# Kernel tuning notes

Measured on AMD Instinct MI355X. Metric: run time of the kernel, lower is better.

## Reference

```python
import jax, jax.numpy as jnp
import numpy as np

N, DEG, F, H, O, B = 100000, 16, 128, 128, 128, 8192


def setup_inputs() -> dict:
    key = jax.random.key(0)
    k1, k2, k3, k4, k5 = jax.random.split(key, 5)
    features = jax.random.normal(k1, (N, F), dtype=jnp.float32)
    w1 = jax.random.normal(k2, (2 * F, H), dtype=jnp.float32)
    w2 = jax.random.normal(k3, (2 * H, O), dtype=jnp.float32)
    neighbor_idx = jax.random.randint(k4, (N, DEG), 0, N, dtype=jnp.int32)
    nodes = jax.random.randint(k5, (B,), 0, N, dtype=jnp.int32)
    return {"features": features, "w1": w1, "w2": w2,
            "neighbor_idx": neighbor_idx, "nodes": nodes}


def reference(features, w1, w2, neighbor_idx, nodes):
    # Layer 1 (computed for all nodes, vectorized): mean-aggregate neighbor
    # raw features, concat with self features, project with w1.
    neigh_feat = features[neighbor_idx]                 # [N, DEG, F] gather
    agg1 = neigh_feat.mean(axis=1)                      # [N, F]
    h1 = jnp.concatenate([features, agg1], axis=-1) @ w1  # [N, H]

    # Layer 2 (batch nodes): mean-aggregate neighbor layer-1 embeddings,
    # concat with self layer-1 embedding, project with w2.
    h1_self = h1[nodes]                                 # [B, H]
    h1_neigh = h1[neighbor_idx[nodes]].mean(axis=1)     # [B, H]
    out = jnp.concatenate([h1_self, h1_neigh], axis=-1) @ w2  # [B, O]
    return out
```

## Files before the change

### kernel.cpp

```cpp
#include <hip/hip_runtime.h>


#define N_NODES 100000
#define DEG     16
#define FDIM    128
#define HDIM    128
#define B_NODES 8192

typedef __attribute__((ext_vector_type(8))) short bf16x8;
typedef __attribute__((ext_vector_type(8))) unsigned short u16x8;
typedef __attribute__((ext_vector_type(4))) float f32x4;
typedef __attribute__((ext_vector_type(2))) float f32x2;

static __device__ __forceinline__ unsigned short f2bf(float f) {
    union { float f; unsigned u; } v; v.f = f;
    unsigned r = v.u + 0x7fff + ((v.u >> 16) & 1);
    return (unsigned short)(r >> 16);
}
static __device__ __forceinline__ float bf2f(unsigned short b) {
    union { unsigned u; float f; } v; v.u = ((unsigned)b) << 16;
    return v.f;
}

__global__ __launch_bounds__(256)
void prep(const float* __restrict__ feat, const float* __restrict__ w1,
          const float* __restrict__ w2, unsigned short* __restrict__ fb,
          unsigned char* __restrict__ f8,
          unsigned short* __restrict__ w1T, unsigned short* __restrict__ w2T) {
    if (blockIdx.x < 6250) {
        long e = ((long)blockIdx.x * 256 + threadIdx.x) * 8;
        float4 v0 = *(const float4*)(feat + e);
        float4 v1 = *(const float4*)(feat + e + 4);
        u16x8 ob;
        ob[0] = f2bf(v0.x); ob[1] = f2bf(v0.y); ob[2] = f2bf(v0.z); ob[3] = f2bf(v0.w);
        ob[4] = f2bf(v1.x); ob[5] = f2bf(v1.y); ob[6] = f2bf(v1.z); ob[7] = f2bf(v1.w);
        *(u16x8*)(fb + e) = ob;
        int p0 = 0, p1 = 0;
        p0 = __builtin_amdgcn_cvt_pk_fp8_f32(v0.x, v0.y, p0, false);
        p0 = __builtin_amdgcn_cvt_pk_fp8_f32(v0.z, v0.w, p0, true);
        p1 = __builtin_amdgcn_cvt_pk_fp8_f32(v1.x, v1.y, p1, false);
        p1 = __builtin_amdgcn_cvt_pk_fp8_f32(v1.z, v1.w, p1, true);
        uint2 o8; o8.x = (unsigned)p0; o8.y = (unsigned)p1;
        *(uint2*)(f8 + e) = o8;
    } else {
        int bid = blockIdx.x - 6250;
        const float* w = (bid < 8) ? w1 : w2;
        unsigned short* wT = (bid < 8) ? w1T : w2T;
        int kb = (bid & 7) * 32;
        int n = threadIdx.x & 127, dk = threadIdx.x >> 7;
#pragma unroll
        for (int i = 0; i < 16; ++i) {
            int k = kb + dk * 16 + i;
            wT[n * 256 + k] = f2bf(w[k * 128 + n]);
        }
    }
}

__global__ __launch_bounds__(256)
void k1_agg(const unsigned char* __restrict__ f8, const int* __restrict__ nbr,
            unsigned short* __restrict__ agg) {
    const int t = threadIdx.x;
    const int node = blockIdx.x * 16 + (t >> 4);
    const int cg = (t & 15) * 8;
    const int* idx = nbr + node * DEG;
    int4 i0 = *(const int4*)(idx);
    int4 i1 = *(const int4*)(idx + 4);
    int4 i2 = *(const int4*)(idx + 8);
    int4 i3 = *(const int4*)(idx + 12);
    int id[16] = {i0.x, i0.y, i0.z, i0.w, i1.x, i1.y, i1.z, i1.w,
                  i2.x, i2.y, i2.z, i2.w, i3.x, i3.y, i3.z, i3.w};
    uint2 v[16];
#pragma unroll
    for (int d = 0; d < DEG; ++d)
        v[d] = *(const uint2*)(f8 + (long)id[d] * FDIM + cg);
    float s[8] = {0.f, 0.f, 0.f, 0.f, 0.f, 0.f, 0.f, 0.f};
#pragma unroll
    for (int d = 0; d < DEG; ++d) {
        f32x2 a0 = __builtin_amdgcn_cvt_pk_f32_fp8((int)v[d].x, false);
        f32x2 a1 = __builtin_amdgcn_cvt_pk_f32_fp8((int)v[d].x, true);
        f32x2 a2 = __builtin_amdgcn_cvt_pk_f32_fp8((int)v[d].y, false);
        f32x2 a3 = __builtin_amdgcn_cvt_pk_f32_fp8((int)v[d].y, true);
        s[0] += a0[0]; s[1] += a0[1]; s[2] += a1[0]; s[3] += a1[1];
        s[4] += a2[0]; s[5] += a2[1]; s[6] += a3[0]; s[7] += a3[1];
    }
    u16x8 o;
#pragma unroll
    for (int j = 0; j < 8; ++j) o[j] = f2bf(s[j] * 0.0625f);
    *(u16x8*)(agg + node * 128 + cg) = o;
}

#define LOAD_CHUNK(BUF, CIDX)                                                        \
    do {                                                                             \
        const int r0_ = row0 + (CIDX) * 32;                                          \
        _Pragma("unroll")                                                            \
        for (int mt_ = 0; mt_ < 2; ++mt_) {                                          \
            int grow_ = r0_ + mt_ * 16 + m16;                                        \
            bool ok_ = grow_ < N_NODES;                                              \
            const unsigned short* pf_ = fb + (long)grow_ * 128 + quad * 8;           \
            const unsigned short* pa_ = agg + (long)grow_ * 128 + quad * 8;          \
            bf16x8 z_ = {};                                                          \
            _Pragma("unroll")                                                        \
            for (int kc_ = 0; kc_ < 4; ++kc_)                                        \
                BUF[mt_][kc_] = ok_ ? *(const bf16x8*)(pf_ + kc_ * 32) : z_;         \
            _Pragma("unroll")                                                        \
            for (int kc_ = 0; kc_ < 4; ++kc_)                                        \
                BUF[mt_][4 + kc_] = ok_ ? *(const bf16x8*)(pa_ + kc_ * 32) : z_;     \
        }                                                                            \
    } while (0)

__global__ __launch_bounds__(256, 2)
void g1(const unsigned short* __restrict__ fb, const unsigned short* __restrict__ agg,
        const unsigned short* __restrict__ w1T, unsigned short* __restrict__ h1) {
    __shared__ unsigned short W[128][264];
    const int t = threadIdx.x, wave = t >> 6, lane = t & 63;
    const int m16 = lane & 15, quad = lane >> 4;
    const int row0 = blockIdx.x * 256;
    const int n0 = wave * 32;

#pragma unroll
    for (int i = 0; i < 16; ++i) {
        int e = i * 2048 + t * 8;
        int n = e >> 8, k = e & 255;
        *(u16x8*)(&W[n][k]) = *(const u16x8*)(w1T + e);
    }
    __syncthreads();

    bf16x8 A0[2][8], A1[2][8], A2[2][8];
    LOAD_CHUNK(A0, 0);
    LOAD_CHUNK(A1, 1);

#pragma unroll
    for (int c = 0; c < 8; ++c) {
        if (c < 6) {
            if ((c % 3) == 0)      LOAD_CHUNK(A2, c + 2);
            else if ((c % 3) == 1) LOAD_CHUNK(A0, c + 2);
            else                   LOAD_CHUNK(A1, c + 2);
        }
        f32x4 acc[2][2] = {};
#pragma unroll
        for (int kc = 0; kc < 8; ++kc) {
            bf16x8 b0 = *(const bf16x8*)(&W[n0 + m16][kc * 32 + quad * 8]);
            bf16x8 b1 = *(const bf16x8*)(&W[n0 + 16 + m16][kc * 32 + quad * 8]);
            bf16x8 a0, a1;
            if ((c % 3) == 0)      { a0 = A0[0][kc]; a1 = A0[1][kc]; }
            else if ((c % 3) == 1) { a0 = A1[0][kc]; a1 = A1[1][kc]; }
            else                   { a0 = A2[0][kc]; a1 = A2[1][kc]; }
            acc[0][0] = __builtin_amdgcn_mfma_f32_16x16x32_bf16(a0, b0, acc[0][0], 0, 0, 0);
            acc[1][0] = __builtin_amdgcn_mfma_f32_16x16x32_bf16(a1, b0, acc[1][0], 0, 0, 0);
            acc[0][1] = __builtin_amdgcn_mfma_f32_16x16x32_bf16(a0, b1, acc[0][1], 0, 0, 0);
            acc[1][1] = __builtin_amdgcn_mfma_f32_16x16x32_bf16(a1, b1, acc[1][1], 0, 0, 0);
        }
        const int r0 = row0 + c * 32;
#pragma unroll
        for (int mt = 0; mt < 2; ++mt)
#pragma unroll
            for (int reg = 0; reg < 4; ++reg) {
                int grow = r0 + mt * 16 + quad * 4 + reg;
                if (grow >= N_NODES) continue;
#pragma unroll
                for (int nt = 0; nt < 2; ++nt)
                    h1[grow * HDIM + n0 + nt * 16 + m16] = f2bf(acc[mt][nt][reg]);
            }
    }
}

__global__ __launch_bounds__(256)
void g2_fused(const unsigned short* __restrict__ h1, const unsigned short* __restrict__ w2T,
              const int* __restrict__ nbr, const int* __restrict__ nodes,
              float* __restrict__ out) {
    __shared__ unsigned short X2[64][264];
    const int t = threadIdx.x, wave = t >> 6, lane = t & 63;
    const int m16 = lane & 15, quad = lane >> 4;
    const int b0 = blockIdx.x * 64;
    const int colb = m16 * 8;

    for (int g = 0; g < 4; ++g) {
        int Ln = wave * 16 + g * 4 + quad;
        int node = nodes[b0 + Ln];
        *(u16x8*)(&X2[Ln][colb]) = *(const u16x8*)(h1 + node * HDIM + colb);
        const int* idx = nbr + node * DEG;
        float s[8] = {0.f, 0.f, 0.f, 0.f, 0.f, 0.f, 0.f, 0.f};
#pragma unroll
        for (int d = 0; d < DEG; ++d) {
            int nb = idx[d];
            u16x8 v = *(const u16x8*)(h1 + nb * HDIM + colb);
#pragma unroll
            for (int j = 0; j < 8; ++j) s[j] += bf2f(v[j]);
        }
        u16x8 o;
#pragma unroll
        for (int j = 0; j < 8; ++j) o[j] = f2bf(s[j] * 0.0625f);
        *(u16x8*)(&X2[Ln][128 + colb]) = o;
    }
    __syncthreads();

    f32x4 acc[8] = {};
#pragma unroll
    for (int kc = 0; kc < 8; ++kc) {
        bf16x8 a = *(const bf16x8*)(&X2[wave * 16 + m16][kc * 32 + quad * 8]);
#pragma unroll
        for (int nt = 0; nt < 8; ++nt) {
            bf16x8 b = *(const bf16x8*)(w2T + (nt * 16 + m16) * 256 + kc * 32 + quad * 8);
            acc[nt] = __builtin_amdgcn_mfma_f32_16x16x32_bf16(a, b, acc[nt], 0, 0, 0);
        }
    }

#pragma unroll
    for (int nt = 0; nt < 8; ++nt)
#pragma unroll
        for (int reg = 0; reg < 4; ++reg) {
            int row = b0 + wave * 16 + quad * 4 + reg;
            out[row * 128 + nt * 16 + m16] = acc[nt][reg];
        }
}

extern "C" void kernel_launch(void* const* d_in, const int* in_sizes, int n_in,
                              void* d_out, int out_size, void* d_ws, size_t ws_size,
                              hipStream_t stream) {
    const float* feat  = (const float*)d_in[0];
    const float* w1    = (const float*)d_in[1];
    const float* w2    = (const float*)d_in[2];
    const int*   nbr   = (const int*)d_in[3];
    const int*   nodes = (const int*)d_in[4];
    float* out = (float*)d_out;

    char* ws = (char*)d_ws;
    unsigned short* fb  = (unsigned short*)ws;
    unsigned char*  f8  = (unsigned char*)(ws + 25600000);
    unsigned short* agg = (unsigned short*)(ws + 38400000);
    unsigned short* h1  = (unsigned short*)(ws + 64000000);
    unsigned short* w1T = (unsigned short*)(ws + 89600000);
    unsigned short* w2T = (unsigned short*)(ws + 89665536);

    prep<<<6266, 256, 0, stream>>>(feat, w1, w2, fb, f8, w1T, w2T);
    k1_agg<<<6250, 256, 0, stream>>>(f8, nbr, agg);
    g1<<<(N_NODES + 255) / 256, 256, 0, stream>>>(fb, agg, w1T, h1);
    g2_fused<<<B_NODES / 64, 256, 0, stream>>>(h1, w2T, nbr, nodes, out);
}
```

Measured before the change: 193.9 us.

## Slice fp8 features by column and restage g1 GEMM through LDS

Prep now writes the fp8 feature copy as four 32-column slices, and k1_agg is remapped so that groups of blocks gather from a single slice. This shrinks the gather working set per slice so it fits better in cache. Separately, g1 is rewritten to use 128-row tiles, with A and W K-chunks streamed into double-buffered LDS via global_load_lds and each wave computing the full 128-column output. The new g1 syncs once per K step and reloads W per chunk instead of keeping it resident in LDS, and g1 rows past N_NODES are read without bounds guards.

```diff
diff --git a/kernel.cpp b/kernel.cpp
--- a/kernel.cpp
+++ b/kernel.cpp
@@ -25,7 +25,7 @@
 __global__ __launch_bounds__(256)
 void prep(const float* __restrict__ feat, const float* __restrict__ w1,
           const float* __restrict__ w2, unsigned short* __restrict__ fb,
-          unsigned char* __restrict__ f8,
+          unsigned char* __restrict__ f8s,
           unsigned short* __restrict__ w1T, unsigned short* __restrict__ w2T) {
     if (blockIdx.x < 6250) {
         long e = ((long)blockIdx.x * 256 + threadIdx.x) * 8;
@@ -40,8 +40,11 @@
         p0 = __builtin_amdgcn_cvt_pk_fp8_f32(v0.z, v0.w, p0, true);
         p1 = __builtin_amdgcn_cvt_pk_fp8_f32(v1.x, v1.y, p1, false);
         p1 = __builtin_amdgcn_cvt_pk_fp8_f32(v1.z, v1.w, p1, true);
+        int node = (int)(e >> 7), col = (int)(e & 127);
+        int slice = col >> 5;
+        unsigned char* dst = f8s + (long)slice * (N_NODES * 32) + (long)node * 32 + (col & 31);
         uint2 o8; o8.x = (unsigned)p0; o8.y = (unsigned)p1;
-        *(uint2*)(f8 + e) = o8;
+        *(uint2*)dst = o8;
     } else {
         int bid = blockIdx.x - 6250;
         const float* w = (bid < 8) ? w1 : w2;
@@ -57,11 +60,15 @@
 }
 
 __global__ __launch_bounds__(256)
-void k1_agg(const unsigned char* __restrict__ f8, const int* __restrict__ nbr,
+void k1_agg(const unsigned char* __restrict__ f8s, const int* __restrict__ nbr,
             unsigned short* __restrict__ agg) {
-    const int t = threadIdx.x;
-    const int node = blockIdx.x * 16 + (t >> 4);
-    const int cg = (t & 15) * 8;
+    const int t = threadIdx.x, b = blockIdx.x;
+    const int s = (b & 7) >> 1;
+    const int chunk = ((b >> 3) << 1) + (b & 1);
+    const int node = chunk * 64 + (t >> 2);
+    if (node >= N_NODES) return;
+    const int q = t & 3;
+    const unsigned char* base = f8s + (long)s * (N_NODES * 32) + q * 8;
     const int* idx = nbr + node * DEG;
     int4 i0 = *(const int4*)(idx);
     int4 i1 = *(const int4*)(idx + 4);
@@ -72,96 +79,89 @@
     uint2 v[16];
 #pragma unroll
     for (int d = 0; d < DEG; ++d)
-        v[d] = *(const uint2*)(f8 + (long)id[d] * FDIM + cg);
-    float s[8] = {0.f, 0.f, 0.f, 0.f, 0.f, 0.f, 0.f, 0.f};
+        v[d] = *(const uint2*)(base + (long)id[d] * 32);
+    float sm[8] = {0.f, 0.f, 0.f, 0.f, 0.f, 0.f, 0.f, 0.f};
 #pragma unroll
     for (int d = 0; d < DEG; ++d) {
         f32x2 a0 = __builtin_amdgcn_cvt_pk_f32_fp8((int)v[d].x, false);
         f32x2 a1 = __builtin_amdgcn_cvt_pk_f32_fp8((int)v[d].x, true);
         f32x2 a2 = __builtin_amdgcn_cvt_pk_f32_fp8((int)v[d].y, false);
         f32x2 a3 = __builtin_amdgcn_cvt_pk_f32_fp8((int)v[d].y, true);
-        s[0] += a0[0]; s[1] += a0[1]; s[2] += a1[0]; s[3] += a1[1];
-        s[4] += a2[0]; s[5] += a2[1]; s[6] += a3[0]; s[7] += a3[1];
+        sm[0] += a0[0]; sm[1] += a0[1]; sm[2] += a1[0]; sm[3] += a1[1];
+        sm[4] += a2[0]; sm[5] += a2[1]; sm[6] += a3[0]; sm[7] += a3[1];
     }
     u16x8 o;
 #pragma unroll
-    for (int j = 0; j < 8; ++j) o[j] = f2bf(s[j] * 0.0625f);
-    *(u16x8*)(agg + node * 128 + cg) = o;
-}
-
-#define LOAD_CHUNK(BUF, CIDX)                                                        \
-    do {                                                                             \
-        const int r0_ = row0 + (CIDX) * 32;                                          \
-        _Pragma("unroll")                                                            \
-        for (int mt_ = 0; mt_ < 2; ++mt_) {                                          \
-            int grow_ = r0_ + mt_ * 16 + m16;                                        \
-            bool ok_ = grow_ < N_NODES;                                              \
-            const unsigned short* pf_ = fb + (long)grow_ * 128 + quad * 8;           \
-            const unsigned short* pa_ = agg + (long)grow_ * 128 + quad * 8;          \
-            bf16x8 z_ = {};                                                          \
-            _Pragma("unroll")                                                        \
-            for (int kc_ = 0; kc_ < 4; ++kc_)                                        \
-                BUF[mt_][kc_] = ok_ ? *(const bf16x8*)(pf_ + kc_ * 32) : z_;         \
-            _Pragma("unroll")                                                        \
-            for (int kc_ = 0; kc_ < 4; ++kc_)                                        \
-                BUF[mt_][4 + kc_] = ok_ ? *(const bf16x8*)(pa_ + kc_ * 32) : z_;     \
-        }                                                                            \
+    for (int j = 0; j < 8; ++j) o[j] = f2bf(sm[j] * 0.0625f);
+    *(u16x8*)(agg + (long)node * 128 + s * 32 + q * 8) = o;
+}
+
+#define STAGE(KC, BUF)                                                                        \
+    do {                                                                                      \
+        const unsigned short* s0_ = ((KC) < 4) ? (fb + (KC) * 32) : (agg + ((KC) - 4) * 32);  \
+        _Pragma("unroll")                                                                     \
+        for (int j_ = 0; j_ < 2; ++j_) {                                                      \
+            long grow_ = row0 + (t >> 2) + j_ * 64;                                           \
+            const unsigned short* ga_ = s0_ + grow_ * 128 + (t & 3) * 8;                      \
+            __builtin_amdgcn_global_load_lds(                                                 \
+                (const __attribute__((address_space(1))) unsigned int*)ga_,                   \
+                (__attribute__((address_space(3))) unsigned int*)                             \
+                    (&AsS[(BUF) * 4096 + wave * 512 + j_ * 2048 + lane * 8]), 16, 0, 0);      \
+            const unsigned short* gw_ = w1T + ((t >> 2) + j_ * 64) * 256 + (KC) * 32 + (t & 3) * 8; \
+            __builtin_amdgcn_global_load_lds(                                                 \
+                (const __attribute__((address_space(1))) unsigned int*)gw_,                   \
+                (__attribute__((address_space(3))) unsigned int*)                             \
+                    (&WsS[(BUF) * 4096 + wave * 512 + j_ * 2048 + lane * 8]), 16, 0, 0);      \
+        }                                                                                     \
     } while (0)
 
 __global__ __launch_bounds__(256, 2)
 void g1(const unsigned short* __restrict__ fb, const unsigned short* __restrict__ agg,
         const unsigned short* __restrict__ w1T, unsigned short* __restrict__ h1) {
-    __shared__ unsigned short W[128][264];
+    __shared__ unsigned short AsS[2 * 4096];
+    __shared__ unsigned short WsS[2 * 4096];
     const int t = threadIdx.x, wave = t >> 6, lane = t & 63;
     const int m16 = lane & 15, quad = lane >> 4;
-    const int row0 = blockIdx.x * 256;
-    const int n0 = wave * 32;
-
-#pragma unroll
-    for (int i = 0; i < 16; ++i) {
-        int e = i * 2048 + t * 8;
-        int n = e >> 8, k = e & 255;
-        *(u16x8*)(&W[n][k]) = *(const u16x8*)(w1T + e);
-    }
-    __syncthreads();
-
-    bf16x8 A0[2][8], A1[2][8], A2[2][8];
-    LOAD_CHUNK(A0, 0);
-    LOAD_CHUNK(A1, 1);
-
-#pragma unroll
-    for (int c = 0; c < 8; ++c) {
-        if (c < 6) {
-            if ((c % 3) == 0)      LOAD_CHUNK(A2, c + 2);
-            else if ((c % 3) == 1) LOAD_CHUNK(A0, c + 2);
-            else                   LOAD_CHUNK(A1, c + 2);
-        }
-        f32x4 acc[2][2] = {};
-#pragma unroll
-        for (int kc = 0; kc < 8; ++kc) {
-            bf16x8 b0 = *(const bf16x8*)(&W[n0 + m16][kc * 32 + quad * 8]);
-            bf16x8 b1 = *(const bf16x8*)(&W[n0 + 16 + m16][kc * 32 + quad * 8]);
-            bf16x8 a0, a1;
-            if ((c % 3) == 0)      { a0 = A0[0][kc]; a1 = A0[1][kc]; }
-            else if ((c % 3) == 1) { a0 = A1[0][kc]; a1 = A1[1][kc]; }
-            else                   { a0 = A2[0][kc]; a1 = A2[1][kc]; }
-            acc[0][0] = __builtin_amdgcn_mfma_f32_16x16x32_bf16(a0, b0, acc[0][0], 0, 0, 0);
-            acc[1][0] = __builtin_amdgcn_mfma_f32_16x16x32_bf16(a1, b0, acc[1][0], 0, 0, 0);
-            acc[0][1] = __builtin_amdgcn_mfma_f32_16x16x32_bf16(a0, b1, acc[0][1], 0, 0, 0);
-            acc[1][1] = __builtin_amdgcn_mfma_f32_16x16x32_bf16(a1, b1, acc[1][1], 0, 0, 0);
-        }
-        const int r0 = row0 + c * 32;
-#pragma unroll
-        for (int mt = 0; mt < 2; ++mt)
-#pragma unroll
-            for (int reg = 0; reg < 4; ++reg) {
-                int grow = r0 + mt * 16 + quad * 4 + reg;
-                if (grow >= N_NODES) continue;
-#pragma unroll
-                for (int nt = 0; nt < 2; ++nt)
-                    h1[grow * HDIM + n0 + nt * 16 + m16] = f2bf(acc[mt][nt][reg]);
+    const long row0 = (long)blockIdx.x * 128;
+
+    f32x4 acc[2][8] = {};
+    STAGE(0, 0);
+#pragma unroll
+    for (int kc = 0; kc < 8; ++kc) {
+        __syncthreads();
+        if (kc < 7) {
+            switch (kc + 1) {
+                case 1: STAGE(1, 1); break;
+                case 2: STAGE(2, 0); break;
+                case 3: STAGE(3, 1); break;
+                case 4: STAGE(4, 0); break;
+                case 5: STAGE(5, 1); break;
+                case 6: STAGE(6, 0); break;
+                case 7: STAGE(7, 1); break;
             }
-    }
+        }
+        const unsigned short* Ab = &AsS[(kc & 1) * 4096];
+        const unsigned short* Wb = &WsS[(kc & 1) * 4096];
+        bf16x8 a0 = *(const bf16x8*)(Ab + (wave * 32 + m16) * 32 + quad * 8);
+        bf16x8 a1 = *(const bf16x8*)(Ab + (wave * 32 + 16 + m16) * 32 + quad * 8);
+#pragma unroll
+        for (int nt = 0; nt < 8; ++nt) {
+            bf16x8 bv = *(const bf16x8*)(Wb + (nt * 16 + m16) * 32 + quad * 8);
+            acc[0][nt] = __builtin_amdgcn_mfma_f32_16x16x32_bf16(a0, bv, acc[0][nt], 0, 0, 0);
+            acc[1][nt] = __builtin_amdgcn_mfma_f32_16x16x32_bf16(a1, bv, acc[1][nt], 0, 0, 0);
+        }
+    }
+
+#pragma unroll
+    for (int mt = 0; mt < 2; ++mt)
+#pragma unroll
+        for (int reg = 0; reg < 4; ++reg) {
+            long grow = row0 + wave * 32 + mt * 16 + quad * 4 + reg;
+            if (grow >= N_NODES) continue;
+#pragma unroll
+            for (int nt = 0; nt < 8; ++nt)
+                h1[grow * HDIM + nt * 16 + m16] = f2bf(acc[mt][nt][reg]);
+        }
 }
 
 __global__ __launch_bounds__(256)
@@ -226,14 +226,14 @@
 
     char* ws = (char*)d_ws;
     unsigned short* fb  = (unsigned short*)ws;
-    unsigned char*  f8  = (unsigned char*)(ws + 25600000);
+    unsigned char*  f8s = (unsigned char*)(ws + 25600000);
     unsigned short* agg = (unsigned short*)(ws + 38400000);
     unsigned short* h1  = (unsigned short*)(ws + 64000000);
     unsigned short* w1T = (unsigned short*)(ws + 89600000);
     unsigned short* w2T = (unsigned short*)(ws + 89665536);
 
-    prep<<<6266, 256, 0, stream>>>(feat, w1, w2, fb, f8, w1T, w2T);
-    k1_agg<<<6250, 256, 0, stream>>>(f8, nbr, agg);
-    g1<<<(N_NODES + 255) / 256, 256, 0, stream>>>(fb, agg, w1T, h1);
+    prep<<<6266, 256, 0, stream>>>(feat, w1, w2, fb, f8s, w1T, w2T);
+    k1_agg<<<6256, 256, 0, stream>>>(f8s, nbr, agg);
+    g1<<<(N_NODES + 127) / 128, 256, 0, stream>>>(fb, agg, w1T, h1);
     g2_fused<<<B_NODES / 64, 256, 0, stream>>>(h1, w2T, nbr, nodes, out);
 }
```

New measurement: 173.1 us. -10.7%, faster.
